# Performance work log

Measured on AMD Instinct MI355X. Metric: run time of the kernel, lower is better.

## Reference

```python
import jax, jax.numpy as jnp
import numpy as np

B, IN_DIM, OUT_DIM, MV = 8192, 256, 256, 8


def setup_inputs() -> dict:
    key = jax.random.key(0)
    k1, k2 = jax.random.split(key)
    x = jax.random.normal(k1, (B, IN_DIM, MV), dtype=jnp.float32)
    weights = jax.random.normal(k2, (IN_DIM, OUT_DIM, MV), dtype=jnp.float32) * 0.01
    bias = jnp.zeros((OUT_DIM, MV), dtype=jnp.float32)
    return {"x": x, "weights": weights, "bias": bias}


def reference(x, weights, bias):
    # Simplified GA-3D geometric product, summed over in_dim (j), per out_dim (i):
    #   y[..., i, 0] = sum_j x[..., j, 0]*W[j,i,0] + x[..., j, 1]*W[j,i,1] + x[..., j, 2]*W[j,i,2]
    #   y[..., i, 4] = sum_j x[..., j, 1]*W[j,i,2] - x[..., j, 2]*W[j,i,1] + x[..., j, 4]*W[j,i,0]
    #   all other multivector components receive only the bias.
    # Scalar component: dot over first 3 multivector slots.
    c0 = jnp.einsum('bjk,jik->bi', x[..., 0:3], weights[..., 0:3])  # (B, OUT_DIM)
    # Bivector component e23: x1*w2 - x2*w1 + x4*w0.
    xv = jnp.stack([x[..., 1], -x[..., 2], x[..., 4]], axis=-1)          # (B, IN_DIM, 3)
    wv = jnp.stack([weights[..., 2], weights[..., 1], weights[..., 0]], axis=-1)  # (IN_DIM, OUT_DIM, 3)
    c4 = jnp.einsum('bjk,jik->bi', xv, wv)  # (B, OUT_DIM)
    y = jnp.broadcast_to(bias, (x.shape[0],) + bias.shape)  # (B, OUT_DIM, MV)
    y = y.at[..., 0].add(c0).at[..., 4].add(c4)
    return y
```

## Files before the change

kernel.cpp:

```cpp
#include <hip/hip_runtime.h>
#include <hip/hip_bf16.h>

typedef __attribute__((ext_vector_type(4))) float f32x4;
typedef __attribute__((ext_vector_type(8))) short bf16x8;
typedef __attribute__((ext_vector_type(4))) short short4v;

#define AROW 264
#define CS 516

__device__ __forceinline__ short f2bf(float f) {
  __hip_bfloat16 h = __float2bfloat16(f);
  return __builtin_bit_cast(short, h);
}

__global__ __launch_bounds__(256) void ga_prep_B(const float* __restrict__ W,
                                                 short* __restrict__ Bp) {
  const int gid = blockIdx.x * 256 + threadIdx.x;
  const int l  = gid & 63;
  const int cg = (gid >> 6) & 31;
  const int it = gid >> 11;
  const int ln = l & 15, q = l >> 4;
  const int hc = cg >> 4;
  const int i  = (cg & 15) * 16 + ln;
  const int j0 = it * 8 + q * 2;
  const float4* W4 = (const float4*)W;

  bf16x8 o;
#pragma unroll
  for (int jj = 0; jj < 2; ++jj) {
    const float4 wv = W4[((j0 + jj) * 256 + i) * 2];
    if (!hc) {
      o[jj * 4 + 0] = f2bf(wv.x); o[jj * 4 + 1] = f2bf(wv.y);
      o[jj * 4 + 2] = f2bf(wv.z); o[jj * 4 + 3] = 0;
    } else {
      o[jj * 4 + 0] = 0;           o[jj * 4 + 1] = f2bf(wv.z);
      o[jj * 4 + 2] = f2bf(-wv.y); o[jj * 4 + 3] = f2bf(wv.x);
    }
  }
  *(bf16x8*)&Bp[(size_t)gid * 8] = o;
}

__global__ __launch_bounds__(512, 2) void ga_mv_main(
    const float* __restrict__ x, const short* __restrict__ Bp,
    const float* __restrict__ bias, float* __restrict__ y) {
  __shared__ __align__(16) char smem[33088];
  short* Abuf[2] = {(short*)smem, (short*)(smem + 16 * AROW * 2)};
  float* c_lds = (float*)smem;

  const int t = threadIdx.x;
  const int bm = blockIdx.x;
  const int lane = t & 63, w = t >> 6;
  const int ln = lane & 15, qq = lane >> 4;
  const int R0 = bm * 16;

  const int ci = t & 127, rb = t >> 7;
  const int jl = ci >> 1, h2 = ci & 1;
  const float4* x4 = (const float4*)x;
  float4 fr[4];

#define LOADX(qtr)                                                           \
  {                                                                          \
    _Pragma("unroll")                                                        \
    for (int i = 0; i < 4; ++i)                                              \
      fr[i] = x4[(size_t)(R0 + rb + 4 * i) * 512 + (qtr) * 128 + ci];        \
  }

#define PROC(dst)                                                            \
  {                                                                          \
    _Pragma("unroll")                                                        \
    for (int i = 0; i < 4; ++i) {                                            \
      const float c4 = __shfl_xor(fr[i].x, 1, 64);                           \
      if (!h2) {                                                             \
        short4v a;                                                           \
        a[0] = f2bf(fr[i].x); a[1] = f2bf(fr[i].y);                          \
        a[2] = f2bf(fr[i].z); a[3] = f2bf(c4);                               \
        *(short4v*)&(dst)[(rb + 4 * i) * AROW + jl * 4] = a;                 \
      }                                                                      \
    }                                                                        \
  }

  const size_t bbase = (size_t)w * 4 * 512 + lane * 8;
  bf16x8 Bf[2][4];
#define LB(itv, b)                                                           \
  {                                                                          \
    const short* p = Bp + (size_t)(itv) * 32 * 512 + bbase;                  \
    Bf[b][0] = *(const bf16x8*)(p);                                          \
    Bf[b][1] = *(const bf16x8*)(p + 512);                                    \
    Bf[b][2] = *(const bf16x8*)(p + 1024);                                   \
    Bf[b][3] = *(const bf16x8*)(p + 1536);                                   \
  }

  LOADX(0);
  PROC(Abuf[0]);
  __syncthreads();
  LB(0, 0);
  LB(1, 1);
  LOADX(1);

  f32x4 acc[4] = {};

#pragma unroll
  for (int q = 0; q < 4; ++q) {
    const short* Ac = Abuf[q & 1];
#pragma unroll
    for (int tau = 0; tau < 8; ++tau) {
      const int it = q * 8 + tau;
      if (tau == 4 && q < 3) {
        PROC(Abuf[(q + 1) & 1]);
        if (q < 2) LOADX(q + 2);
      }
      const bf16x8 af = *(const bf16x8*)&Ac[ln * AROW + (tau * 8 + qq * 2) * 4];
#pragma unroll
      for (int n = 0; n < 4; ++n)
        acc[n] = __builtin_amdgcn_mfma_f32_16x16x32_bf16(af, Bf[it & 1][n],
                                                         acc[n], 0, 0, 0);
      if (it + 2 < 32) LB(it + 2, it & 1);
    }
    __syncthreads();
  }

#pragma unroll
  for (int n = 0; n < 4; ++n)
#pragma unroll
    for (int r = 0; r < 4; ++r)
      c_lds[(qq * 4 + r) * CS + w * 64 + n * 16 + ln] = acc[n][r];
  __syncthreads();

  const int h = t & 1, p = t >> 1;
  const float4 bv = ((const float4*)bias)[p * 2 + h];
  float4* y4 = (float4*)y;
#pragma unroll
  for (int r = 0; r < 16; ++r) {
    float4 o = bv;
    o.x += c_lds[r * CS + h * 256 + p];
    y4[((size_t)(R0 + r) * 256 + p) * 2 + h] = o;
  }
}

extern "C" void kernel_launch(void* const* d_in, const int* in_sizes, int n_in,
                              void* d_out, int out_size, void* d_ws, size_t ws_size,
                              hipStream_t stream) {
  const float* x = (const float*)d_in[0];
  const float* W = (const float*)d_in[1];
  const float* bias = (const float*)d_in[2];
  float* y = (float*)d_out;
  short* Bp = (short*)d_ws;

  ga_prep_B<<<dim3(256), dim3(256), 0, stream>>>(W, Bp);
  ga_mv_main<<<dim3(512), dim3(512), 0, stream>>>(x, Bp, bias, y);
}
```

Measured before the change: 133.1 us.

## Retile GA GEMM into 64-row by 64-column-group blocks with grouped block ordering

Each block now covers 64 batch rows and a 64-wide slice of the 128 packed output columns instead of 16 rows by all 512, so there are four column groups per row tile. Each wave holds one B fragment and loops over four A row-fragments from LDS. The K loop is pipelined in 16 finer stages with a 4-deep B register ring. Launch bounds rise to 4 blocks per SM, and the block index is swizzled so eight row tiles share a column group for L2 reuse of B. The cost is that x is read four times, once per column group, in exchange for less B traffic per row and higher occupancy.

```diff
diff --git a/kernel.cpp b/kernel.cpp
--- a/kernel.cpp
+++ b/kernel.cpp
@@ -5,8 +5,8 @@
 typedef __attribute__((ext_vector_type(8))) short bf16x8;
 typedef __attribute__((ext_vector_type(4))) short short4v;
 
-#define AROW 264
-#define CS 516
+#define ARS 72
+#define CS 132
 
 __device__ __forceinline__ short f2bf(float f) {
   __hip_bfloat16 h = __float2bfloat16(f);
@@ -17,11 +17,12 @@
                                                  short* __restrict__ Bp) {
   const int gid = blockIdx.x * 256 + threadIdx.x;
   const int l  = gid & 63;
-  const int cg = (gid >> 6) & 31;
+  const int fc = (gid >> 6) & 7;
+  const int cg = (gid >> 9) & 3;
   const int it = gid >> 11;
   const int ln = l & 15, q = l >> 4;
-  const int hc = cg >> 4;
-  const int i  = (cg & 15) * 16 + ln;
+  const int hc = fc >> 2;
+  const int i  = cg * 64 + (fc & 3) * 16 + ln;
   const int j0 = it * 8 + q * 2;
   const float4* W4 = (const float4*)W;
 
@@ -40,100 +41,104 @@
   *(bf16x8*)&Bp[(size_t)gid * 8] = o;
 }
 
-__global__ __launch_bounds__(512, 2) void ga_mv_main(
+__global__ __launch_bounds__(512, 4) void ga_mv_main(
     const float* __restrict__ x, const short* __restrict__ Bp,
     const float* __restrict__ bias, float* __restrict__ y) {
-  __shared__ __align__(16) char smem[33088];
-  short* Abuf[2] = {(short*)smem, (short*)(smem + 16 * AROW * 2)};
+  __shared__ __align__(16) char smem[33792];
+
+  const int t = threadIdx.x;
+  const int id = blockIdx.x;
+  const int g = id & 7;
+  const int cg = (id >> 3) & 3;
+  const int bm = (id >> 5) * 8 + g;
+  const int R0 = bm * 64;
+  const int lane = t & 63, w = t >> 6;
+  const int ln = lane & 15, qq = lane >> 4;
+
+  short* Ab0 = (short*)smem;
+  short* Ab1 = (short*)(smem + 9216);
   float* c_lds = (float*)smem;
 
-  const int t = threadIdx.x;
-  const int bm = blockIdx.x;
-  const int lane = t & 63, w = t >> 6;
-  const int ln = lane & 15, qq = lane >> 4;
-  const int R0 = bm * 16;
-
-  const int ci = t & 127, rb = t >> 7;
-  const int jl = ci >> 1, h2 = ci & 1;
+  const int c32 = t & 31, tb = t >> 5;
+  const int h2 = t & 1;
+  const int jl = c32 >> 1;
   const float4* x4 = (const float4*)x;
   float4 fr[4];
 
-#define LOADX(qtr)                                                           \
-  {                                                                          \
-    _Pragma("unroll")                                                        \
-    for (int i = 0; i < 4; ++i)                                              \
-      fr[i] = x4[(size_t)(R0 + rb + 4 * i) * 512 + (qtr) * 128 + ci];        \
+#define LOADX(s)                                                            \
+  {                                                                         \
+    _Pragma("unroll")                                                       \
+    for (int i = 0; i < 4; ++i)                                             \
+      fr[i] = x4[(size_t)(R0 + i * 16 + tb) * 512 + (s) * 32 + c32];        \
   }
 
-#define PROC(dst)                                                            \
-  {                                                                          \
-    _Pragma("unroll")                                                        \
-    for (int i = 0; i < 4; ++i) {                                            \
-      const float c4 = __shfl_xor(fr[i].x, 1, 64);                           \
-      if (!h2) {                                                             \
-        short4v a;                                                           \
-        a[0] = f2bf(fr[i].x); a[1] = f2bf(fr[i].y);                          \
-        a[2] = f2bf(fr[i].z); a[3] = f2bf(c4);                               \
-        *(short4v*)&(dst)[(rb + 4 * i) * AROW + jl * 4] = a;                 \
-      }                                                                      \
-    }                                                                        \
+#define PROC(dst)                                                           \
+  {                                                                         \
+    _Pragma("unroll")                                                       \
+    for (int i = 0; i < 4; ++i) {                                           \
+      const float c4v = __shfl_xor(fr[i].x, 1, 64);                         \
+      if (!h2) {                                                            \
+        short4v a;                                                          \
+        a[0] = f2bf(fr[i].x); a[1] = f2bf(fr[i].y);                         \
+        a[2] = f2bf(fr[i].z); a[3] = f2bf(c4v);                             \
+        *(short4v*)&(dst)[(i * 16 + tb) * ARS + jl * 4] = a;                \
+      }                                                                     \
+    }                                                                       \
   }
 
-  const size_t bbase = (size_t)w * 4 * 512 + lane * 8;
-  bf16x8 Bf[2][4];
-#define LB(itv, b)                                                           \
-  {                                                                          \
-    const short* p = Bp + (size_t)(itv) * 32 * 512 + bbase;                  \
-    Bf[b][0] = *(const bf16x8*)(p);                                          \
-    Bf[b][1] = *(const bf16x8*)(p + 512);                                    \
-    Bf[b][2] = *(const bf16x8*)(p + 1024);                                   \
-    Bf[b][3] = *(const bf16x8*)(p + 1536);                                   \
+  const short* bpw = Bp + ((size_t)cg * 8 + w) * 512 + lane * 8;
+  bf16x8 Bf[4];
+#define LB(itv) Bf[(itv) & 3] = *(const bf16x8*)(bpw + (size_t)(itv) * 32 * 512);
+
+#define COMPUTE(Ac, tau, bfrag)                                             \
+  {                                                                         \
+    _Pragma("unroll")                                                       \
+    for (int m = 0; m < 4; ++m) {                                           \
+      const bf16x8 af =                                                     \
+          *(const bf16x8*)&(Ac)[(m * 16 + ln) * ARS + (tau) * 32 + qq * 8]; \
+      acc[m] = __builtin_amdgcn_mfma_f32_16x16x32_bf16(af, bfrag, acc[m],   \
+                                                       0, 0, 0);            \
+    }                                                                       \
   }
-
-  LOADX(0);
-  PROC(Abuf[0]);
-  __syncthreads();
-  LB(0, 0);
-  LB(1, 1);
-  LOADX(1);
 
   f32x4 acc[4] = {};
 
+  LOADX(0);
+  PROC(Ab0);
+  LOADX(1);
+  LB(0); LB(1); LB(2); LB(3);
+  __syncthreads();
+
 #pragma unroll
-  for (int q = 0; q < 4; ++q) {
-    const short* Ac = Abuf[q & 1];
-#pragma unroll
-    for (int tau = 0; tau < 8; ++tau) {
-      const int it = q * 8 + tau;
-      if (tau == 4 && q < 3) {
-        PROC(Abuf[(q + 1) & 1]);
-        if (q < 2) LOADX(q + 2);
-      }
-      const bf16x8 af = *(const bf16x8*)&Ac[ln * AROW + (tau * 8 + qq * 2) * 4];
-#pragma unroll
-      for (int n = 0; n < 4; ++n)
-        acc[n] = __builtin_amdgcn_mfma_f32_16x16x32_bf16(af, Bf[it & 1][n],
-                                                         acc[n], 0, 0, 0);
-      if (it + 2 < 32) LB(it + 2, it & 1);
-    }
+  for (int s = 0; s < 16; ++s) {
+    short* Ac = (s & 1) ? Ab1 : Ab0;
+    short* An = (s & 1) ? Ab0 : Ab1;
+    const int it0 = 2 * s;
+    COMPUTE(Ac, 0, Bf[it0 & 3]);
+    if (it0 + 4 < 32) LB(it0 + 4);
+    if (s < 15) PROC(An);
+    if (s < 14) LOADX(s + 2);
+    COMPUTE(Ac, 1, Bf[(it0 + 1) & 3]);
+    if (it0 + 5 < 32) LB(it0 + 5);
     __syncthreads();
   }
 
 #pragma unroll
-  for (int n = 0; n < 4; ++n)
+  for (int m = 0; m < 4; ++m)
 #pragma unroll
     for (int r = 0; r < 4; ++r)
-      c_lds[(qq * 4 + r) * CS + w * 64 + n * 16 + ln] = acc[n][r];
+      c_lds[(m * 16 + qq * 4 + r) * CS + w * 16 + ln] = acc[m][r];
   __syncthreads();
 
-  const int h = t & 1, p = t >> 1;
-  const float4 bv = ((const float4*)bias)[p * 2 + h];
+  const int h = t & 1, p = (t >> 1) & 63, rr = t >> 7;
+  const float4 bv = ((const float4*)bias)[(cg * 64 + p) * 2 + h];
   float4* y4 = (float4*)y;
 #pragma unroll
-  for (int r = 0; r < 16; ++r) {
+  for (int r0 = 0; r0 < 16; ++r0) {
+    const int row = r0 * 4 + rr;
     float4 o = bv;
-    o.x += c_lds[r * CS + h * 256 + p];
-    y4[((size_t)(R0 + r) * 256 + p) * 2 + h] = o;
+    o.x += c_lds[row * CS + h * 64 + p];
+    y4[((size_t)(R0 + row) * 256 + cg * 64 + p) * 2 + h] = o;
   }
 }
 
```

Measured after the change: 142.4 us. 1.07x slower.
